# Performance work log

Hardware: AMD Instinct MI355X
Metric: run time of the kernel (lower is better)

Reference implementation:

```python
import jax, jax.numpy as jnp
import numpy as np

EMBED = 384
HEADS = 7
HEAD_SIZE = EMBED // HEADS  # 54; concat dim = 378 != 384 (faithful to source)
SEQ = 512
BATCH = 64
FFN = 6 * EMBED
EPS = 1e-5


def _layernorm(x, g, b):
    mu = jnp.mean(x, axis=-1, keepdims=True)
    var = jnp.mean((x - mu) ** 2, axis=-1, keepdims=True)
    return (x - mu) * jax.lax.rsqrt(var + EPS) * g + b


def setup_inputs() -> dict:
    key = jax.random.key(0)
    ks = jax.random.split(key, 14)
    s = 0.02
    return {
        "x": jax.random.normal(ks[0], (BATCH, SEQ, EMBED), jnp.float32),
        # per-head q/k/v projections stacked over heads: [H, EMBED, HEAD_SIZE]
        "wq": jax.random.normal(ks[1], (HEADS, EMBED, HEAD_SIZE), jnp.float32) * s,
        "bq": jnp.zeros((HEADS, HEAD_SIZE), jnp.float32),
        "wk": jax.random.normal(ks[2], (HEADS, EMBED, HEAD_SIZE), jnp.float32) * s,
        "bk": jnp.zeros((HEADS, HEAD_SIZE), jnp.float32),
        "wv": jax.random.normal(ks[3], (HEADS, EMBED, HEAD_SIZE), jnp.float32) * s,
        "bv": jnp.zeros((HEADS, HEAD_SIZE), jnp.float32),
        "wo": jax.random.normal(ks[4], (HEADS * HEAD_SIZE, EMBED), jnp.float32) * s,
        "bo": jnp.zeros((EMBED,), jnp.float32),
        "w1": jax.random.normal(ks[5], (EMBED, FFN), jnp.float32) * s,
        "b1": jnp.zeros((FFN,), jnp.float32),
        "w2": jax.random.normal(ks[6], (FFN, EMBED), jnp.float32) * s,
        "b2": jnp.zeros((EMBED,), jnp.float32),
        "ln1_g": jnp.ones((EMBED,), jnp.float32),
        "ln1_b": jnp.zeros((EMBED,), jnp.float32),
        "ln2_g": jnp.ones((EMBED,), jnp.float32),
        "ln2_b": jnp.zeros((EMBED,), jnp.float32),
    }


def reference(x, wq, bq, wk, bk, wv, bv, wo, bo, w1, b1, w2, b2, ln1_g, ln1_b, ln2_g, ln2_b):
    B, S, D = x.shape
    # --- multi-head causal self-attention (pre-LN) ---
    h = _layernorm(x, ln1_g, ln1_b)
    q = jnp.einsum("bsd,hdk->bhsk", h, wq) + bq[None, :, None, :]
    k = jnp.einsum("bsd,hdk->bhsk", h, wk) + bk[None, :, None, :]
    v = jnp.einsum("bsd,hdk->bhsk", h, wv) + bv[None, :, None, :]
    scale = HEAD_SIZE ** -0.5
    scores = jnp.einsum("bhsk,bhtk->bhst", q, k) * scale  # [B,H,S,S]
    causal = jnp.tril(jnp.ones((S, S), dtype=bool))
    scores = jnp.where(causal, scores, jnp.float32(-jnp.inf))
    attn = jax.nn.softmax(scores, axis=-1)
    o = jnp.einsum("bhst,bhtk->bhsk", attn, v)  # [B,H,S,hs]
    o = jnp.transpose(o, (0, 2, 1, 3)).reshape(B, S, HEADS * HEAD_SIZE)
    x = x + o @ wo + bo  # dropout = identity (eval)
    # --- feed-forward (pre-LN), exact GELU ---
    h2 = _layernorm(x, ln2_g, ln2_b)
    ff = jax.nn.gelu(h2 @ w1 + b1, approximate=False) @ w2 + b2
    return x + ff
```

## Files before the change

### kernel.cpp

```cpp
#include <hip/hip_runtime.h>
#include <hip/hip_bf16.h>
#include <cmath>

#define BATCH 64
#define SEQ   512
#define EMBED 384
#define HEADS 7
#define HSZ   54
#define FFND  2304
#define NTOK  (BATCH*SEQ)
#define QKVN  1152
#define EPS   1e-5f
#define LAM   0.19632593f
#define THR2  11.5415603f

typedef __attribute__((ext_vector_type(8))) short s16x8;
typedef __attribute__((ext_vector_type(4))) float f32x4;

__device__ __forceinline__ ushort f2bf(float f) {
  __hip_bfloat16 h = __float2bfloat16(f);
  return *reinterpret_cast<ushort*>(&h);
}

__device__ __forceinline__ float exp2fast(float f) {
  return __builtin_amdgcn_exp2f(f);
}

__device__ __forceinline__ void gload16(const void* g, void* l) {
  __builtin_amdgcn_global_load_lds((const __attribute__((address_space(1))) void*)g,
                                   (__attribute__((address_space(3))) void*)l, 16, 0, 0);
}

__global__ __launch_bounds__(256) void ln_bf16_kernel(const float* __restrict__ x,
    const float* __restrict__ g, const float* __restrict__ b, ushort* __restrict__ out) {
  int wave = threadIdx.x >> 6, lane = threadIdx.x & 63;
  int row = (blockIdx.x << 2) + wave;
  const float* xr = x + (size_t)row * EMBED;
  float v[6]; float s = 0.f;
#pragma unroll
  for (int i = 0; i < 6; ++i) { v[i] = xr[lane + (i << 6)]; s += v[i]; }
#pragma unroll
  for (int off = 32; off; off >>= 1) s += __shfl_xor(s, off);
  float mu = s * (1.f / EMBED);
  float var = 0.f;
#pragma unroll
  for (int i = 0; i < 6; ++i) { float d = v[i] - mu; var += d * d; }
#pragma unroll
  for (int off = 32; off; off >>= 1) var += __shfl_xor(var, off);
  float rstd = rsqrtf(var * (1.f / EMBED) + EPS);
  ushort* orow = out + (size_t)row * EMBED;
#pragma unroll
  for (int i = 0; i < 6; ++i) {
    int c = lane + (i << 6);
    orow[c] = f2bf((v[i] - mu) * rstd * g[c] + b[c]);
  }
}

__device__ __forceinline__ void convT_body(const float* __restrict__ in,
    ushort* __restrict__ out, int K, int N, int srcK, int srcN,
    int k0, int n0, int tid, float (*t)[33]) {
  int tx = tid & 31, ty = tid >> 5;
#pragma unroll
  for (int i = 0; i < 4; ++i) {
    int r = ty + i * 8;
    int k = k0 + r, n = n0 + tx;
    t[r][tx] = (k < srcK && n < srcN) ? in[(size_t)k * srcN + n] : 0.f;
  }
  __syncthreads();
#pragma unroll
  for (int i = 0; i < 4; ++i) {
    int r = ty + i * 8;
    int n = n0 + r, k = k0 + tx;
    if (n < N && k < K) out[(size_t)n * K + k] = f2bf(t[tx][r]);
  }
}

__global__ __launch_bounds__(256) void prep_all(
    const float* __restrict__ wq, const float* __restrict__ wk, const float* __restrict__ wv,
    const float* __restrict__ bq, const float* __restrict__ bk, const float* __restrict__ bv,
    const float* __restrict__ wo, const float* __restrict__ w1, const float* __restrict__ w2,
    ushort* __restrict__ wqkvt, ushort* __restrict__ wot,
    ushort* __restrict__ w1t, ushort* __restrict__ w2t,
    float* __restrict__ bqkv, ushort* __restrict__ aout) {
  __shared__ float t[32][33];
  int bid = blockIdx.x, tid = threadIdx.x;
  if (bid < 504) {
    int z = bid / 24, rem = bid - z * 24;
    int k0 = (rem >> 1) << 5, hs0 = (rem & 1) << 5;
    int type = z / 7, h = z - type * 7;
    const float* W = (type == 0) ? wq : (type == 1) ? wk : wv;
    float lam = (type == 0) ? LAM : 1.f;
    int tx = tid & 31, ty = tid >> 5;
#pragma unroll
    for (int i = 0; i < 4; ++i) {
      int r = ty + i * 8;
      int k = k0 + r, hs = hs0 + tx;
      t[r][tx] = (hs < HSZ) ? W[((size_t)h * EMBED + k) * HSZ + hs] : 0.f;
    }
    __syncthreads();
#pragma unroll
    for (int i = 0; i < 4; ++i) {
      int r = ty + i * 8;
      int hs = hs0 + r;
      if (hs < HSZ)
        wqkvt[(size_t)(type * 378 + h * HSZ + hs) * EMBED + k0 + tx] = f2bf(t[tx][r] * lam);
    }
  } else if (bid < 531) {
    int idx = (bid - 504) * 256 + tid;
    if (idx < 18 * EMBED) wqkvt[1134 * EMBED + idx] = 0;
    if (idx < QKVN) {
      float bval = 0.f;
      if (idx < 1134) {
        int type = idx / 378, rem = idx - type * 378;
        int h = rem / HSZ, hs = rem - h * HSZ;
        const float* B = (type == 0) ? bq : (type == 1) ? bk : bv;
        bval = B[h * HSZ + hs];
        if (type == 0) bval *= LAM;
      }
      bqkv[idx] = bval;
    }
  } else if (bid < 675) {
    int r = bid - 531;
    convT_body(wo, wot, EMBED, EMBED, 378, EMBED, (r / 12) << 5, (r % 12) << 5, tid, t);
  } else if (bid < 1539) {
    int r = bid - 675;
    convT_body(w1, w1t, EMBED, FFND, EMBED, FFND, (r % 12) << 5, (r / 12) << 5, tid, t);
  } else if (bid < 2403) {
    int r = bid - 1539;
    convT_body(w2, w2t, FFND, EMBED, FFND, EMBED, (r % 72) << 5, (r / 72) << 5, tid, t);
  } else {
    int idx = (bid - 2403) * 256 + tid;
    if (idx < NTOK * 6) {
      int row = idx / 6, c = idx - row * 6;
      aout[(size_t)row * EMBED + 378 + c] = 0;
    }
  }
}

__global__ __launch_bounds__(512) void attn_mfma_kernel(const ushort* __restrict__ qkv,
    ushort* __restrict__ o) {
  __shared__ ushort S[16384];
  int tid = threadIdx.x;
  int id = blockIdx.x;
  int xcd = id & 7;
  int sseq = id >> 3;
  int bh = xcd + 8 * (sseq >> 2);
  int qb = 3 - (sseq & 3);
  int b = bh / HEADS, h = bh - b * HEADS;
  int qr0 = qb << 7;
  int ntile = 2 * qb + 2;
  int w = tid >> 6, l = tid & 63;
  int lr = l & 15, lg = l >> 4;
  const ushort* base = qkv + (size_t)b * SEQ * QKVN + h * HSZ;
  const size_t TSTR = (size_t)64 * QKVN * 2;

  int grow = w * 8 + (l >> 3);
  int gc = (l & 7) ^ (l >> 3);
  const char* kg  = (const char*)(base + 378 + (size_t)grow * QKVN + gc * 8);
  const char* qg0 = (const char*)(base + (size_t)(qr0 + grow) * QKVN + gc * 8);
  const char* qg1 = (const char*)(base + (size_t)(qr0 + 64 + grow) * QKVN + gc * 8);
  int vdst[4]; const char* vsrc[4]; bool vpar[4];
#pragma unroll
  for (int i = 0; i < 4; ++i) {
    int e = tid + i * 512;
    int ev = e >> 1, par = e & 1;
    int p = ev / 28, cv = ev - p * 28;
    if (cv < 27 && p < 32) {
      int k0 = 2 * p;
      int s0 = ((k0 >> 5) << 5) | (((k0 >> 2) & 3) << 3) | (((k0 >> 4) & 1) << 2) | (k0 & 3);
      int d = 2 * cv + par;
      vdst[i] = d * 64 + (s0 ^ ((d & 7) << 3));
      vsrc[i] = (const char*)(base + 756 + (size_t)(2 * p + par) * QKVN + 2 * cv);
      vpar[i] = (par != 0);
    } else { vdst[i] = -1; vsrc[i] = (const char*)base; vpar[i] = false; }
  }

  gload16(qg0, (char*)S + 16384 + w * 1024);
  gload16(qg1, (char*)S + 24576 + w * 1024);
  gload16(kg, (char*)S + w * 1024);
  uint uv[4];
#pragma unroll
  for (int i = 0; i < 4; ++i)
    uv[i] = (vdst[i] >= 0) ? *reinterpret_cast<const uint*>(vsrc[i]) : 0u;
  __syncthreads();
  for (int e = tid; e < 640; e += 512) {
    int r = e / 5, which = e - r * 5;
    int idx = (which == 0) ? (r * 64 + ((6 ^ (r & 7)) << 3) + 6)
                           : (r * 64 + ((7 ^ (r & 7)) << 3) + 2 * (which - 1));
    *reinterpret_cast<uint*>(&S[8192 + idx]) = 0;
  }
#pragma unroll
  for (int i = 0; i < 4; ++i) {
    uint u = uv[i]; uint uo = __shfl_xor(u, 1);
    if (vdst[i] >= 0) {
      uint wv2 = vpar[i] ? ((uo >> 16) | (u & 0xffff0000u)) : ((u & 0xffffu) | (uo << 16));
      *reinterpret_cast<uint*>(&S[4096 + vdst[i]]) = wv2;
    }
  }
  __syncthreads();
  int qrow = w * 16 + lr;
  s16x8 qf[2];
  qf[0] = *reinterpret_cast<const s16x8*>(&S[8192 + qrow * 64 + ((8 * lg) ^ ((qrow & 7) << 3))]);
  qf[1] = *reinterpret_cast<const s16x8*>(&S[8192 + qrow * 64 + ((32 + 8 * lg) ^ ((qrow & 7) << 3))]);
  __syncthreads();

  int qglob = qr0 + qrow;
  float mrow = -1e30f, lrow = 0.f;
  f32x4 acc[4];
#pragma unroll
  for (int d = 0; d < 4; ++d) acc[d] = (f32x4){0.f, 0.f, 0.f, 0.f};

  for (int kt = 0; kt < ntile; ++kt) {
    int cur = kt & 1, nxt = cur ^ 1;
    int curo = cur * 8192;
    if (kt + 1 < ntile) {
      kg += TSTR;
      gload16(kg, (char*)S + nxt * 16384 + w * 1024);
#pragma unroll
      for (int i = 0; i < 4; ++i) {
        vsrc[i] += TSTR;
        if (vdst[i] >= 0) uv[i] = *reinterpret_cast<const uint*>(vsrc[i]);
      }
    }
    bool active = (kt * 64) <= (qr0 + w * 16 + 15);
    if (active) {
      bool diag = (kt * 64 + 63) > (qr0 + w * 16);
      f32x4 sacc[4];
      __builtin_amdgcn_s_setprio(1);
#pragma unroll
      for (int kb = 0; kb < 4; ++kb) {
        sacc[kb] = (f32x4){0.f, 0.f, 0.f, 0.f};
#pragma unroll
        for (int h2 = 0; h2 < 2; ++h2) {
          int row = kb * 16 + lr;
          s16x8 kf = *reinterpret_cast<const s16x8*>(
              &S[curo + row * 64 + ((32 * h2 + 8 * lg) ^ ((row & 7) << 3))]);
          sacc[kb] = __builtin_amdgcn_mfma_f32_16x16x32_bf16(kf, qf[h2], sacc[kb], 0, 0, 0);
        }
      }
      __builtin_amdgcn_s_setprio(0);
      float sv[4][4];
      float mt = -1e30f;
#pragma unroll
      for (int kb = 0; kb < 4; ++kb)
#pragma unroll
        for (int r = 0; r < 4; ++r) {
          float s = sacc[kb][r];
          if (diag && (kt * 64 + kb * 16 + 4 * lg + r) > qglob) s = -1e30f;
          sv[kb][r] = s;
          mt = fmaxf(mt, s);
        }
      mt = fmaxf(mt, __shfl_xor(mt, 16));
      mt = fmaxf(mt, __shfl_xor(mt, 32));
      if (!__all(mt - mrow <= THR2)) {
        float mnew = fmaxf(mrow, mt);
        float al = exp2fast(mrow - mnew);
#pragma unroll
        for (int d = 0; d < 4; ++d)
#pragma unroll
          for (int r = 0; r < 4; ++r) acc[d][r] *= al;
        lrow *= al;
        mrow = mnew;
      }
      union { short s[16]; s16x8 v[2]; } pp;
      float lsum = 0.f;
#pragma unroll
      for (int kb = 0; kb < 4; ++kb)
#pragma unroll
        for (int r = 0; r < 4; ++r) {
          float p = exp2fast(sv[kb][r] - mrow);
          lsum += p;
          pp.s[kb * 4 + r] = (short)f2bf(p);
        }
      lrow += lsum;
      __builtin_amdgcn_s_setprio(1);
#pragma unroll
      for (int m = 0; m < 2; ++m)
#pragma unroll
        for (int d = 0; d < 4; ++d) {
          int row = d * 16 + lr;
          s16x8 vf = *reinterpret_cast<const s16x8*>(
              &S[curo + 4096 + row * 64 + ((32 * m + 8 * lg) ^ ((row & 7) << 3))]);
          acc[d] = __builtin_amdgcn_mfma_f32_16x16x32_bf16(vf, pp.v[m], acc[d], 0, 0, 0);
        }
      __builtin_amdgcn_s_setprio(0);
    }
    if (kt + 1 < ntile) {
#pragma unroll
      for (int i = 0; i < 4; ++i) {
        uint u = uv[i]; uint uo = __shfl_xor(u, 1);
        if (vdst[i] >= 0) {
          uint wv2 = vpar[i] ? ((uo >> 16) | (u & 0xffff0000u)) : ((u & 0xffffu) | (uo << 16));
          *reinterpret_cast<uint*>(&S[nxt * 8192 + 4096 + vdst[i]]) = wv2;
        }
      }
      __syncthreads();
    }
  }

  lrow += __shfl_xor(lrow, 16);
  lrow += __shfl_xor(lrow, 32);
  float linv = 1.f / lrow;
  ushort* Olds = S;
#pragma unroll
  for (int d = 0; d < 4; ++d)
#pragma unroll
    for (int r = 0; r < 4; ++r)
      Olds[(d * 16 + 4 * lg + r) * 128 + w * 16 + lr] = f2bf(acc[d][r] * linv);
  __syncthreads();
  for (int e = tid; e < 128 * 27; e += 512) {
    int q = e / 27, c = e - q * 27;
    uint lo = Olds[(2 * c) * 128 + q];
    uint hi = Olds[(2 * c + 1) * 128 + q];
    *reinterpret_cast<uint*>(&o[(size_t)(b * SEQ + qr0 + q) * EMBED + h * HSZ + 2 * c]) =
        lo | (hi << 16);
  }
}

template<int KSTEPS, int LDA, int LDB, int MODE, int NY>
__global__ __launch_bounds__(256) void mfma_gemm(
    const char* __restrict__ Ab, const char* __restrict__ Btb,
    const float* __restrict__ bias, const float* __restrict__ resid,
    char* __restrict__ Cb, int ncols) {
  __shared__ ushort sh[32768];
  int tid = threadIdx.x;
  int id = blockIdx.x;
  int xcd = id & 7, t = id >> 3;
  int group = t / (4 * NY), rres = t - group * (4 * NY);
  int ytile = rres >> 2, xi = rres & 3;
  int tok0 = (xcd * 32 + group * 4 + xi) << 7;
  int col0 = ytile << 7;
  int wv = tid >> 6, l = tid & 63;
  int wr = wv >> 1, wc = wv & 1;
  int lr = l & 15, lg = l >> 4;

  const char* aptr[4]; const char* bptr[4];
#pragma unroll
  for (int is = 0; is < 4; ++is) {
    int i = is * 256 + tid;
    int row = i >> 3;
    int boff = (i & 7) << 4;
    int sw = boff ^ ((row & 7) << 4);
    aptr[is] = Ab + (size_t)(tok0 + row) * LDA + sw;
    bptr[is] = Btb + (size_t)(col0 + row) * LDB + sw;
  }

  int offA[2][4], offB[2][4];
#pragma unroll
  for (int m = 0; m < 4; ++m) {
    int rowa = wr * 64 + m * 16 + lr;
    int rowb = wc * 64 + m * 16 + lr;
    int sa = (rowa & 7) << 4, sb = (rowb & 7) << 4;
#pragma unroll
    for (int kk = 0; kk < 2; ++kk) {
      int kb = kk * 64 + lg * 16;
      offA[kk][m] = (rowa * 128 + (kb ^ sa)) >> 1;
      offB[kk][m] = (rowb * 128 + (kb ^ sb)) >> 1;
    }
  }

  f32x4 acc[4][4];
#pragma unroll
  for (int m = 0; m < 4; ++m)
#pragma unroll
    for (int n = 0; n < 4; ++n) acc[m][n] = (f32x4){0.f, 0.f, 0.f, 0.f};

#pragma unroll
  for (int is = 0; is < 4; ++is) {
    gload16(aptr[is], (char*)sh + is * 4096 + wv * 1024);
    gload16(bptr[is], (char*)sh + 32768 + is * 4096 + wv * 1024);
  }
  __syncthreads();

  for (int ks = 0; ks < KSTEPS; ++ks) {
    int buf = ks & 1;
    if (ks + 1 < KSTEPS) {
      int nb = buf ^ 1;
#pragma unroll
      for (int is = 0; is < 4; ++is) {
        gload16(aptr[is] + (size_t)(ks + 1) * 128, (char*)sh + nb * 16384 + is * 4096 + wv * 1024);
        gload16(bptr[is] + (size_t)(ks + 1) * 128, (char*)sh + 32768 + nb * 16384 + is * 4096 + wv * 1024);
      }
    }
    int ao = buf * 8192, bo = 16384 + buf * 8192;
    __builtin_amdgcn_s_setprio(1);
#pragma unroll
    for (int kk = 0; kk < 2; ++kk) {
      s16x8 af[4], bfr[4];
#pragma unroll
      for (int m = 0; m < 4; ++m) af[m] = *reinterpret_cast<const s16x8*>(&sh[ao + offA[kk][m]]);
#pragma unroll
      for (int n = 0; n < 4; ++n) bfr[n] = *reinterpret_cast<const s16x8*>(&sh[bo + offB[kk][n]]);
#pragma unroll
      for (int m = 0; m < 4; ++m)
#pragma unroll
        for (int n = 0; n < 4; ++n)
          acc[m][n] = __builtin_amdgcn_mfma_f32_16x16x32_bf16(af[m], bfr[n], acc[m][n], 0, 0, 0);
    }
    __builtin_amdgcn_s_setprio(0);
    if (ks + 1 < KSTEPS) __syncthreads();
  }

  float bn[4];
  int colr = col0 + wc * 64 + lr;
#pragma unroll
  for (int n = 0; n < 4; ++n) bn[n] = bias[colr + n * 16];

  if constexpr (MODE == 2) {
    int tokr = tok0 + wr * 64 + lg * 4;
    float* C = (float*)Cb;
#pragma unroll
    for (int m = 0; m < 4; ++m)
#pragma unroll
      for (int r = 0; r < 4; ++r) {
        size_t rowbase = (size_t)(tokr + m * 16 + r) * ncols;
#pragma unroll
        for (int n = 0; n < 4; ++n) {
          size_t idx = rowbase + colr + n * 16;
          C[idx] = acc[m][n][r] + bn[n] + resid[idx];
        }
      }
  } else {
    __syncthreads();
#pragma unroll
    for (int m = 0; m < 4; ++m)
#pragma unroll
      for (int r = 0; r < 4; ++r) {
        int row = wr * 64 + m * 16 + lg * 4 + r;
        int rmask = ((row >> 2) & 3) << 4;
#pragma unroll
        for (int n = 0; n < 4; ++n) {
          float xg = acc[m][n][r] + bn[n];
          if constexpr (MODE == 1) {
            float u2 = xg * (2.3022082f + 0.10294324f * xg * xg);
            xg = xg * __builtin_amdgcn_rcpf(1.f + exp2fast(-u2));
          }
          int col = wc * 64 + n * 16 + lr;
          sh[row * 128 + (col ^ rmask)] = f2bf(xg);
        }
      }
    __syncthreads();
    ushort* C = (ushort*)Cb;
    int blk = (l & 7) + 8 * (wv & 1);
    int rbase = (l >> 3) + 64 * (wv >> 1);
#pragma unroll
    for (int it = 0; it < 8; ++it) {
      int row = rbase + 8 * it;
      int pblk = blk ^ (((row >> 2) & 3) << 1);
      uint4 vvv = *reinterpret_cast<const uint4*>(&sh[row * 128 + pblk * 8]);
      *reinterpret_cast<uint4*>(&C[(size_t)(tok0 + row) * ncols + col0 + blk * 8]) = vvv;
    }
  }
}

extern "C" void kernel_launch(void* const* d_in, const int* in_sizes, int n_in,
                              void* d_out, int out_size, void* d_ws, size_t ws_size,
                              hipStream_t stream) {
  const float* x    = (const float*)d_in[0];
  const float* wq   = (const float*)d_in[1];
  const float* bq   = (const float*)d_in[2];
  const float* wk   = (const float*)d_in[3];
  const float* bk   = (const float*)d_in[4];
  const float* wv   = (const float*)d_in[5];
  const float* bv   = (const float*)d_in[6];
  const float* wo   = (const float*)d_in[7];
  const float* bo   = (const float*)d_in[8];
  const float* w1   = (const float*)d_in[9];
  const float* b1   = (const float*)d_in[10];
  const float* w2   = (const float*)d_in[11];
  const float* b2   = (const float*)d_in[12];
  const float* ln1g = (const float*)d_in[13];
  const float* ln1b = (const float*)d_in[14];
  const float* ln2g = (const float*)d_in[15];
  const float* ln2b = (const float*)d_in[16];
  float* out = (float*)d_out;

  char* wsb = (char*)d_ws;
  float*  x1    = (float*)wsb;
  ushort* ffnb  = (ushort*)(wsb + 50331648);
  ushort* hb    = (ushort*)(wsb + 50331648);
  ushort* qkvb  = (ushort*)(wsb + 75497472);
  ushort* aout  = (ushort*)(wsb + 150994944);
  ushort* h2b   = (ushort*)(wsb + 201326592);
  ushort* w1t   = (ushort*)(wsb + 226492416);
  ushort* w2t   = (ushort*)(wsb + 228261888);
  ushort* wqkvt = (ushort*)(wsb + 230031360);
  ushort* wot   = (ushort*)(wsb + 230916096);
  float*  bqkv  = (float*)(wsb + 231211008);

  prep_all<<<3171, 256, 0, stream>>>(wq, wk, wv, bq, bk, bv, wo, w1, w2,
                                     wqkvt, wot, w1t, w2t, bqkv, aout);
  ln_bf16_kernel<<<NTOK / 4, 256, 0, stream>>>(x, ln1g, ln1b, hb);
  mfma_gemm<EMBED / 64, EMBED * 2, EMBED * 2, 0, QKVN / 128>
      <<<256 * (QKVN / 128), 256, 0, stream>>>(
      (const char*)hb, (const char*)wqkvt, bqkv, nullptr, (char*)qkvb, QKVN);
  attn_mfma_kernel<<<BATCH * HEADS * 4, 512, 0, stream>>>(qkvb, aout);
  mfma_gemm<EMBED / 64, EMBED * 2, EMBED * 2, 2, EMBED / 128>
      <<<256 * (EMBED / 128), 256, 0, stream>>>(
      (const char*)aout, (const char*)wot, bo, x, (char*)x1, EMBED);
  ln_bf16_kernel<<<NTOK / 4, 256, 0, stream>>>(x1, ln2g, ln2b, h2b);
  mfma_gemm<EMBED / 64, EMBED * 2, EMBED * 2, 1, FFND / 128>
      <<<256 * (FFND / 128), 256, 0, stream>>>(
      (const char*)h2b, (const char*)w1t, b1, nullptr, (char*)ffnb, FFND);
  mfma_gemm<FFND / 64, FFND * 2, FFND * 2, 2, EMBED / 128>
      <<<256 * (EMBED / 128), 256, 0, stream>>>(
      (const char*)ffnb, (const char*)w2t, b2, x1, (char*)out, EMBED);
}
```

Measured before the change: 347.0 us.

## Fuse FFN up-projection, GELU and down-projection into one kernel

Replaces the two FFN GEMM launches with a single kernel in which each 128-token block computes 128-column chunks of the hidden activation, applies GELU, keeps the chunk in LDS as bf16 and immediately accumulates it into the 384-wide output with W2 tiles. This removes the write and re-read of the 32768x2304 bf16 intermediate in global memory and one kernel launch. In exchange, the grid shrinks to 256 blocks of 512 threads with a large LDS footprint and many accumulator registers, and the A tile is reloaded for every FFN chunk, so occupancy and load balance may suffer.

```diff
diff --git a/kernel.cpp b/kernel.cpp
--- a/kernel.cpp
+++ b/kernel.cpp
@@ -451,6 +451,189 @@
       *reinterpret_cast<uint4*>(&C[(size_t)(tok0 + row) * ncols + col0 + blk * 8]) = vvv;
     }
   }
+}
+
+#define B2BASE0 32768
+#define B2BASE1 48128
+#define B2BASE2 0
+#define B2BASE3 16384
+#define PBAS    63488
+
+__global__ __launch_bounds__(512, 2) void ffn_fused(
+    const ushort* __restrict__ h2b, const ushort* __restrict__ w1t,
+    const ushort* __restrict__ w2t, const float* __restrict__ b1,
+    const float* __restrict__ b2, const float* __restrict__ x1,
+    float* __restrict__ out) {
+  __shared__ ushort FS[79872];
+  int tid = threadIdx.x;
+  int id = blockIdx.x;
+  int xcd = id & 7;
+  int tok0 = (xcd * 32 + (id >> 3)) << 7;
+  int w = tid >> 6, l = tid & 63;
+  int wm = w >> 1, wn = w & 1;
+  int lr = l & 15, lg = l >> 4;
+
+  int arow = tid >> 3;
+  int acs = (tid & 7) ^ (arow & 7);
+  const ushort* aS0 = h2b + (size_t)(tok0 + arow) * 384 + acs * 8;
+  const ushort* aS1 = h2b + (size_t)(tok0 + arow + 64) * 384 + acs * 8;
+  const ushort* bS0 = w1t + (size_t)arow * 384 + acs * 8;
+  const ushort* bS1 = w1t + (size_t)(arow + 64) * 384 + acs * 8;
+  int b2r[4], b2q[4];
+#pragma unroll
+  for (int s = 0; s < 4; ++s) {
+    int i = tid + s * 512;
+    int r = i / 5, c = i - r * 5;
+    b2r[s] = (r < 384) ? r : 383;
+    b2q[s] = (c < 4) ? c : 3;
+  }
+
+  int offA1[2][2], offPf[2][4], offB1f[4][2], offB2f[12];
+#pragma unroll
+  for (int mf = 0; mf < 2; ++mf) {
+    int row = wm * 32 + mf * 16 + lr;
+#pragma unroll
+    for (int k = 0; k < 2; ++k)
+      offA1[mf][k] = row * 64 + (((k * 4 + lg) ^ (row & 7)) << 3);
+#pragma unroll
+    for (int k = 0; k < 4; ++k)
+      offPf[mf][k] = PBAS + row * 128 + (((k * 4 + lg) ^ (row & 7)) << 3);
+  }
+#pragma unroll
+  for (int nf = 0; nf < 4; ++nf) {
+    int row = wn * 64 + nf * 16 + lr;
+#pragma unroll
+    for (int k = 0; k < 2; ++k)
+      offB1f[nf][k] = row * 64 + (((k * 4 + lg) ^ (row & 7)) << 3);
+  }
+#pragma unroll
+  for (int nf = 0; nf < 12; ++nf)
+    offB2f[nf] = (wn * 192 + nf * 16 + lr) * 40 + lg * 8;
+
+  f32x4 acc2[2][12];
+#pragma unroll
+  for (int a = 0; a < 2; ++a)
+#pragma unroll
+    for (int bn = 0; bn < 12; ++bn) acc2[a][bn] = (f32x4){0.f, 0.f, 0.f, 0.f};
+
+#define STAGE_A1(KS, BASE) do { \
+    gload16(aS0 + (KS) * 64, (char*)FS + (BASE) * 2 + tid * 16); \
+    gload16(aS1 + (KS) * 64, (char*)FS + (BASE) * 2 + tid * 16 + 8192); } while (0)
+#define STAGE_B1(W1OFF, KS, BASE) do { \
+    gload16(bS0 + (W1OFF) + (KS) * 64, (char*)FS + (BASE) * 2 + tid * 16); \
+    gload16(bS1 + (W1OFF) + (KS) * 64, (char*)FS + (BASE) * 2 + tid * 16 + 8192); } while (0)
+#define STAGE_B2(FC, K2, BASE) do { \
+    _Pragma("unroll") \
+    for (int s_ = 0; s_ < 4; ++s_) { \
+      if (s_ < 3 || tid < 384) \
+        gload16(w2t + (size_t)b2r[s_] * 2304 + (FC) * 128 + (K2) * 32 + b2q[s_] * 8, \
+                (char*)FS + (BASE) * 2 + (tid + s_ * 512) * 16); \
+    } } while (0)
+
+  STAGE_A1(0, 0);
+  STAGE_B1(0, 0, 16384);
+  STAGE_B2(0, 0, B2BASE0);
+  __syncthreads();
+
+  for (int fc = 0; fc < 18; ++fc) {
+    size_t w1off = (size_t)fc * 49152;
+    f32x4 pacc[2][4];
+#pragma unroll
+    for (int a = 0; a < 2; ++a)
+#pragma unroll
+      for (int bn = 0; bn < 4; ++bn) pacc[a][bn] = (f32x4){0.f, 0.f, 0.f, 0.f};
+
+    for (int ks = 0; ks < 6; ++ks) {
+      int ab = (ks & 1) ? 8192 : 0;
+      int bb = (ks & 1) ? 24576 : 16384;
+      if (ks < 5) {
+        int na = (ks & 1) ? 0 : 8192;
+        int nb = (ks & 1) ? 16384 : 24576;
+        STAGE_A1(ks + 1, na);
+        STAGE_B1(w1off, ks + 1, nb);
+      }
+      if (ks == 0) STAGE_B2(fc, 1, B2BASE1);
+      __builtin_amdgcn_s_setprio(1);
+#pragma unroll
+      for (int k = 0; k < 2; ++k) {
+        s16x8 af[2], bf[4];
+#pragma unroll
+        for (int mf = 0; mf < 2; ++mf)
+          af[mf] = *reinterpret_cast<const s16x8*>(&FS[ab + offA1[mf][k]]);
+#pragma unroll
+        for (int nf = 0; nf < 4; ++nf)
+          bf[nf] = *reinterpret_cast<const s16x8*>(&FS[bb + offB1f[nf][k]]);
+#pragma unroll
+        for (int mf = 0; mf < 2; ++mf)
+#pragma unroll
+          for (int nf = 0; nf < 4; ++nf)
+            pacc[mf][nf] = __builtin_amdgcn_mfma_f32_16x16x32_bf16(af[mf], bf[nf], pacc[mf][nf], 0, 0, 0);
+      }
+      __builtin_amdgcn_s_setprio(0);
+      __syncthreads();
+    }
+    STAGE_B2(fc, 2, B2BASE2);
+    STAGE_B2(fc, 3, B2BASE3);
+    float b1v[4];
+#pragma unroll
+    for (int nf = 0; nf < 4; ++nf) b1v[nf] = b1[fc * 128 + wn * 64 + nf * 16 + lr];
+#pragma unroll
+    for (int mf = 0; mf < 2; ++mf)
+#pragma unroll
+      for (int nf = 0; nf < 4; ++nf)
+#pragma unroll
+        for (int r = 0; r < 4; ++r) {
+          float xg = pacc[mf][nf][r] + b1v[nf];
+          float u2 = xg * (2.3022082f + 0.10294324f * xg * xg);
+          xg = xg * __builtin_amdgcn_rcpf(1.f + exp2fast(-u2));
+          int prow = wm * 32 + mf * 16 + 4 * lg + r;
+          int pcol = wn * 64 + nf * 16 + lr;
+          FS[PBAS + prow * 128 + ((((pcol >> 3) ^ (prow & 7))) << 3) + (pcol & 7)] = f2bf(xg);
+        }
+    __syncthreads();
+    __builtin_amdgcn_s_setprio(1);
+#pragma unroll
+    for (int k2 = 0; k2 < 4; ++k2) {
+      const int b2b = (k2 == 0) ? B2BASE0 : (k2 == 1) ? B2BASE1 : (k2 == 2) ? B2BASE2 : B2BASE3;
+      s16x8 af2[2];
+#pragma unroll
+      for (int mf = 0; mf < 2; ++mf)
+        af2[mf] = *reinterpret_cast<const s16x8*>(&FS[offPf[mf][k2]]);
+      s16x8 bf2[12];
+#pragma unroll
+      for (int nf = 0; nf < 12; ++nf)
+        bf2[nf] = *reinterpret_cast<const s16x8*>(&FS[b2b + offB2f[nf]]);
+#pragma unroll
+      for (int mf = 0; mf < 2; ++mf)
+#pragma unroll
+        for (int nf = 0; nf < 12; ++nf)
+          acc2[mf][nf] = __builtin_amdgcn_mfma_f32_16x16x32_bf16(af2[mf], bf2[nf], acc2[mf][nf], 0, 0, 0);
+    }
+    __builtin_amdgcn_s_setprio(0);
+    __syncthreads();
+    if (fc < 17) {
+      STAGE_A1(0, 0);
+      STAGE_B1(w1off + 49152, 0, 16384);
+      STAGE_B2(fc + 1, 0, B2BASE0);
+    }
+    __syncthreads();
+  }
+
+  float bn2[12];
+#pragma unroll
+  for (int nf = 0; nf < 12; ++nf) bn2[nf] = b2[wn * 192 + nf * 16 + lr];
+#pragma unroll
+  for (int mf = 0; mf < 2; ++mf)
+#pragma unroll
+    for (int r = 0; r < 4; ++r) {
+      int row = tok0 + wm * 32 + mf * 16 + 4 * lg + r;
+      size_t rowbase = (size_t)row * EMBED;
+#pragma unroll
+      for (int nf = 0; nf < 12; ++nf) {
+        size_t idx = rowbase + wn * 192 + nf * 16 + lr;
+        out[idx] = acc2[mf][nf][r] + bn2[nf] + x1[idx];
+      }
+    }
 }
 
 extern "C" void kernel_launch(void* const* d_in, const int* in_sizes, int n_in,
@@ -477,7 +660,6 @@
 
   char* wsb = (char*)d_ws;
   float*  x1    = (float*)wsb;
-  ushort* ffnb  = (ushort*)(wsb + 50331648);
   ushort* hb    = (ushort*)(wsb + 50331648);
   ushort* qkvb  = (ushort*)(wsb + 75497472);
   ushort* aout  = (ushort*)(wsb + 150994944);
@@ -499,10 +681,5 @@
       <<<256 * (EMBED / 128), 256, 0, stream>>>(
       (const char*)aout, (const char*)wot, bo, x, (char*)x1, EMBED);
   ln_bf16_kernel<<<NTOK / 4, 256, 0, stream>>>(x1, ln2g, ln2b, h2b);
-  mfma_gemm<EMBED / 64, EMBED * 2, EMBED * 2, 1, FFND / 128>
-      <<<256 * (FFND / 128), 256, 0, stream>>>(
-      (const char*)h2b, (const char*)w1t, b1, nullptr, (char*)ffnb, FFND);
-  mfma_gemm<FFND / 64, FFND * 2, FFND * 2, 2, EMBED / 128>
-      <<<256 * (EMBED / 128), 256, 0, stream>>>(
-      (const char*)ffnb, (const char*)w2t, b2, x1, (char*)out, EMBED);
-}
+  ffn_fused<<<NTOK / 128, 512, 0, stream>>>(h2b, w1t, w2t, b1, b2, x1, out);
+}
```

Result: slower. 372.3 us (+7.3%).

## Fuse FFN up-projection, GELU and down-projection into one kernel

Applied to the files above, without the earlier changes.

Replaces the two separate FFN GEMM launches with a single kernel. Each 64-token block computes 128-column chunks of h2@w1, applies bias and GELU, and stages the bf16 result in LDS. It then immediately accumulates that chunk's contribution to the down-projection in registers, so the 32768x2304 intermediate is never written to or read back from global memory. In exchange, the w1 tiles are reloaded for every token block and the w2 fragments are read directly from global memory without LDS staging. Only 512 blocks are launched, and each holds 48 accumulator registers per lane, which limits occupancy.

```diff
diff --git a/kernel.cpp b/kernel.cpp
--- a/kernel.cpp
+++ b/kernel.cpp
@@ -449,6 +449,142 @@
       int pblk = blk ^ (((row >> 2) & 3) << 1);
       uint4 vvv = *reinterpret_cast<const uint4*>(&sh[row * 128 + pblk * 8]);
       *reinterpret_cast<uint4*>(&C[(size_t)(tok0 + row) * ncols + col0 + blk * 8]) = vvv;
+    }
+  }
+}
+
+#define FA0 0
+#define FA1 4096
+#define FB0 8192
+#define FB1 16384
+#define FP  24576
+
+__global__ __launch_bounds__(512, 4) void ffn_fused(
+    const ushort* __restrict__ h2b, const ushort* __restrict__ w1t,
+    const ushort* __restrict__ w2t, const float* __restrict__ b1,
+    const float* __restrict__ b2, const float* __restrict__ x1,
+    float* __restrict__ out) {
+  __shared__ ushort FS[32768];
+  int tid = threadIdx.x;
+  int id = blockIdx.x;
+  int xcd = id & 7;
+  int tok0 = (xcd * 64 + (id >> 3)) << 6;
+  int w = tid >> 6, l = tid & 63;
+  int wm = w >> 1, wn = w & 1;
+  int lr = l & 15, lg = l >> 4;
+
+  int srow = tid >> 3;
+  int schk = (tid & 7) ^ (srow & 7);
+  const ushort* aS   = h2b + (size_t)(tok0 + srow) * 384 + schk * 8;
+  const ushort* b1S0 = w1t + (size_t)srow * 384 + schk * 8;
+  const ushort* b1S1 = w1t + (size_t)(srow + 64) * 384 + schk * 8;
+  const ushort* w2base = w2t + (size_t)(wn * 192 + lr) * 2304 + lg * 8;
+
+  int arow = wm * 16 + lr;
+  int offA[2], offP[4];
+#pragma unroll
+  for (int kk = 0; kk < 2; ++kk)
+    offA[kk] = arow * 64 + (((kk * 4 + lg) ^ (arow & 7)) << 3);
+#pragma unroll
+  for (int k2 = 0; k2 < 4; ++k2)
+    offP[k2] = FP + arow * 128 + (((k2 * 4 + lg) ^ (arow & 7)) << 3);
+  int offB1[4][2];
+#pragma unroll
+  for (int nf = 0; nf < 4; ++nf) {
+    int row = wn * 64 + nf * 16 + lr;
+#pragma unroll
+    for (int kk = 0; kk < 2; ++kk)
+      offB1[nf][kk] = row * 64 + (((kk * 4 + lg) ^ (row & 7)) << 3);
+  }
+
+  f32x4 acc2[12];
+#pragma unroll
+  for (int nf = 0; nf < 12; ++nf) acc2[nf] = (f32x4){0.f, 0.f, 0.f, 0.f};
+
+#define STAGE_A(KS, BASE) \
+    gload16(aS + (KS) * 64, (char*)FS + (BASE) * 2 + tid * 16)
+#define STAGE_B(FCO, KS, BASE) do { \
+    gload16(b1S0 + (FCO) + (KS) * 64, (char*)FS + (BASE) * 2 + tid * 16); \
+    gload16(b1S1 + (FCO) + (KS) * 64, (char*)FS + (BASE) * 2 + 8192 + tid * 16); } while (0)
+
+  STAGE_A(0, FA0);
+  STAGE_B(0, 0, FB0);
+  __syncthreads();
+
+  for (int fc = 0; fc < 18; ++fc) {
+    size_t w1off = (size_t)fc * 128 * 384;
+    f32x4 pacc[4];
+#pragma unroll
+    for (int nf = 0; nf < 4; ++nf) pacc[nf] = (f32x4){0.f, 0.f, 0.f, 0.f};
+
+    for (int ks = 0; ks < 6; ++ks) {
+      int ab = (ks & 1) ? FA1 : FA0;
+      int bb = (ks & 1) ? FB1 : FB0;
+      if (ks < 5) {
+        STAGE_A(ks + 1, (ks & 1) ? FA0 : FA1);
+        STAGE_B(w1off, ks + 1, (ks & 1) ? FB0 : FB1);
+      }
+      __builtin_amdgcn_s_setprio(1);
+#pragma unroll
+      for (int kk = 0; kk < 2; ++kk) {
+        s16x8 af = *reinterpret_cast<const s16x8*>(&FS[ab + offA[kk]]);
+        s16x8 bf[4];
+#pragma unroll
+        for (int nf = 0; nf < 4; ++nf)
+          bf[nf] = *reinterpret_cast<const s16x8*>(&FS[bb + offB1[nf][kk]]);
+#pragma unroll
+        for (int nf = 0; nf < 4; ++nf)
+          pacc[nf] = __builtin_amdgcn_mfma_f32_16x16x32_bf16(af, bf[nf], pacc[nf], 0, 0, 0);
+      }
+      __builtin_amdgcn_s_setprio(0);
+      if (ks < 5) __syncthreads();
+    }
+    float b1v[4];
+#pragma unroll
+    for (int nf = 0; nf < 4; ++nf) b1v[nf] = b1[fc * 128 + wn * 64 + nf * 16 + lr];
+#pragma unroll
+    for (int nf = 0; nf < 4; ++nf)
+#pragma unroll
+      for (int r = 0; r < 4; ++r) {
+        float xg = pacc[nf][r] + b1v[nf];
+        float u2 = xg * (2.3022082f + 0.10294324f * xg * xg);
+        xg = xg * __builtin_amdgcn_rcpf(1.f + exp2fast(-u2));
+        int prow = wm * 16 + 4 * lg + r;
+        int pcol = wn * 64 + nf * 16 + lr;
+        FS[FP + prow * 128 + (((pcol >> 3) ^ (prow & 7)) << 3) + (pcol & 7)] = f2bf(xg);
+      }
+    __syncthreads();
+    if (fc < 17) {
+      STAGE_A(0, FA0);
+      STAGE_B(w1off + 49152, 0, FB0);
+    }
+#pragma unroll
+    for (int k2 = 0; k2 < 4; ++k2) {
+      s16x8 af2 = *reinterpret_cast<const s16x8*>(&FS[offP[k2]]);
+      s16x8 bf2[12];
+#pragma unroll
+      for (int nf = 0; nf < 12; ++nf)
+        bf2[nf] = *reinterpret_cast<const s16x8*>(w2base + (size_t)nf * 16 * 2304 + fc * 128 + k2 * 32);
+      __builtin_amdgcn_s_setprio(1);
+#pragma unroll
+      for (int nf = 0; nf < 12; ++nf)
+        acc2[nf] = __builtin_amdgcn_mfma_f32_16x16x32_bf16(af2, bf2[nf], acc2[nf], 0, 0, 0);
+      __builtin_amdgcn_s_setprio(0);
+    }
+    __syncthreads();
+  }
+
+  float bn2[12];
+#pragma unroll
+  for (int nf = 0; nf < 12; ++nf) bn2[nf] = b2[wn * 192 + nf * 16 + lr];
+#pragma unroll
+  for (int r = 0; r < 4; ++r) {
+    int row = tok0 + wm * 16 + 4 * lg + r;
+    size_t rowbase = (size_t)row * EMBED;
+#pragma unroll
+    for (int nf = 0; nf < 12; ++nf) {
+      size_t idx = rowbase + wn * 192 + nf * 16 + lr;
+      out[idx] = acc2[nf][r] + bn2[nf] + x1[idx];
     }
   }
 }
@@ -477,7 +613,6 @@
 
   char* wsb = (char*)d_ws;
   float*  x1    = (float*)wsb;
-  ushort* ffnb  = (ushort*)(wsb + 50331648);
   ushort* hb    = (ushort*)(wsb + 50331648);
   ushort* qkvb  = (ushort*)(wsb + 75497472);
   ushort* aout  = (ushort*)(wsb + 150994944);
@@ -499,10 +634,5 @@
       <<<256 * (EMBED / 128), 256, 0, stream>>>(
       (const char*)aout, (const char*)wot, bo, x, (char*)x1, EMBED);
   ln_bf16_kernel<<<NTOK / 4, 256, 0, stream>>>(x1, ln2g, ln2b, h2b);
-  mfma_gemm<EMBED / 64, EMBED * 2, EMBED * 2, 1, FFND / 128>
-      <<<256 * (FFND / 128), 256, 0, stream>>>(
-      (const char*)h2b, (const char*)w1t, b1, nullptr, (char*)ffnb, FFND);
-  mfma_gemm<FFND / 64, FFND * 2, FFND * 2, 2, EMBED / 128>
-      <<<256 * (EMBED / 128), 256, 0, stream>>>(
-      (const char*)ffnb, (const char*)w2t, b2, x1, (char*)out, EMBED);
-}
+  ffn_fused<<<512, 512, 0, stream>>>(h2b, w1t, w2t, b1, b2, x1, out);
+}
```

After: 793.4 us. 129% more time.
